# Kernel optimization log

Measured on AMD Instinct MI355X. Metric: run time of the kernel, lower is better.

## Reference

```python
import jax, jax.numpy as jnp
import numpy as np

NEG_SLOPE = 0.01  # torch LeakyReLU default


def setup_inputs() -> dict:
    N, H, Da, A, E, T, M = 100000, 256, 128, 250000, 60000, 512, 20000
    key = jax.random.key(0)
    ks = jax.random.split(key, 10)
    inp = {
        "nodes_representations": jax.random.normal(ks[0], (N, H), dtype=jnp.float32),
        "hyperedge_arg_node_idxs": jax.random.randint(ks[1], (A,), 0, N),
        "unq_hyperedge_type_reprs": jax.random.normal(ks[2], (T, H), dtype=jnp.float32),
        "hyperedge_type_name_unq_idxs": jax.random.randint(ks[3], (E,), 0, T),
        "unq_hyperedge_arg_name_reprs": jax.random.normal(ks[4], (M, Da), dtype=jnp.float32),
        "hyperedge_arg_name_unq_idxs": jax.random.randint(ks[5], (A,), 0, M),
        "hyperedge_arg_to_edge_id": jax.random.randint(ks[6], (A,), 0, E),
        "num_edges": E,
        "W1": jax.random.normal(ks[7], (H + Da, H), dtype=jnp.float32) * 0.05,
        "b1": jnp.zeros((H,), dtype=jnp.float32),
        "W2": jax.random.normal(ks[8], (2 * H + Da, H), dtype=jnp.float32) * 0.05,
        "b2": jnp.zeros((H,), dtype=jnp.float32),
    }
    return inp


def reference(nodes_representations, hyperedge_arg_node_idxs, unq_hyperedge_type_reprs,
              hyperedge_type_name_unq_idxs, unq_hyperedge_arg_name_reprs,
              hyperedge_arg_name_unq_idxs, hyperedge_arg_to_edge_id, num_edges,
              W1, b1, W2, b2):
    # Gather per-arg name and node reprs, concat -> [A, Da+H]
    arg_name = unq_hyperedge_arg_name_reprs[hyperedge_arg_name_unq_idxs]
    arg_node = nodes_representations[hyperedge_arg_node_idxs]
    arg_reprs = jnp.concatenate([arg_name, arg_node], axis=-1)

    Da = arg_name.shape[1]
    # Edge type reprs [E, H], zero-padded to [E, H+Da] (branch always taken here)
    edge_type = unq_hyperedge_type_reprs[hyperedge_type_name_unq_idxs]
    edge_type = jnp.concatenate(
        [edge_type, jnp.zeros((edge_type.shape[0], Da), dtype=edge_type.dtype)], axis=-1)

    # Message MLP on stacked [A+E, H+Da]
    all_in = jnp.concatenate([arg_reprs, edge_type], axis=0)
    msgs = jax.nn.leaky_relu(all_in @ W1 + b1, negative_slope=NEG_SLOPE)

    # Segment-max grouped by edge id (every edge gets its own type message, so no empty segments)
    seg_ids = jnp.concatenate(
        [hyperedge_arg_to_edge_id, jnp.arange(num_edges, dtype=hyperedge_arg_to_edge_id.dtype)])
    edge_states = jax.ops.segment_max(msgs, seg_ids, num_segments=num_edges)

    # Update MLP: gather edge state per arg, concat with arg reprs -> [A, 2H+Da]
    # (Dropout is identity in eval mode.)
    upd_in = jnp.concatenate([edge_states[hyperedge_arg_to_edge_id], arg_reprs], axis=1)
    message_to_nodes = jax.nn.leaky_relu(upd_in @ W2 + b2, negative_slope=NEG_SLOPE)
    return (message_to_nodes, edge_states)
```

## Files before the change

kernel.cpp:

```cpp
#include <hip/hip_runtime.h>
#include <stdint.h>

#define A_CNT 250000
#define E_CNT 60000
#define H_DIM 256
#define DA    128
#define K1    384
#define K2    640
#define NEG_SLOPE 0.01f
#define SENT  0xFFFFFFFFu
#define XS    40

typedef float v4f __attribute__((ext_vector_type(4)));
typedef short v8s __attribute__((ext_vector_type(8)));
typedef unsigned short u16;

__device__ __forceinline__ unsigned enc_f(float f) {
    unsigned u = __float_as_uint(f);
    return (u & 0x80000000u) ? ~u : (u | 0x80000000u);
}
__device__ __forceinline__ float dec_f(unsigned e) {
    unsigned u = (e & 0x80000000u) ? (e & 0x7FFFFFFFu) : ~e;
    return __uint_as_float(u);
}
__device__ __forceinline__ u16 f2bf(float f) {
    unsigned u = __float_as_uint(f);
    u += 0x7FFFu + ((u >> 16) & 1u);
    return (u16)(u >> 16);
}
__device__ __forceinline__ uint4 pack8(float4 a, float4 b) {
    union { u16 u[8]; uint4 v; } p;
    p.u[0]=f2bf(a.x); p.u[1]=f2bf(a.y); p.u[2]=f2bf(a.z); p.u[3]=f2bf(a.w);
    p.u[4]=f2bf(b.x); p.u[5]=f2bf(b.y); p.u[6]=f2bf(b.z); p.u[7]=f2bf(b.w);
    return p.v;
}

__global__ void wprep_kernel(const float* __restrict__ W, u16* __restrict__ Wt, int K) {
    int k = blockIdx.x, c = threadIdx.x;
    Wt[(size_t)c * K + k] = f2bf(W[(size_t)k * 256 + c]);
}

__global__ void hist_kernel(const int* __restrict__ arg_edge, unsigned* __restrict__ counts) {
    int i = blockIdx.x * 256 + threadIdx.x;
    if (i < A_CNT) atomicAdd(&counts[arg_edge[i]], 1u);
}

__global__ __launch_bounds__(1024) void scan_kernel(const unsigned* __restrict__ counts,
                                                    unsigned* __restrict__ cursor) {
    __shared__ unsigned sd[1024];
    const int tid = threadIdx.x;
    const int CH = (E_CNT + 1023) / 1024;
    const int base = tid * CH;
    unsigned s = 0;
    for (int i = 0; i < CH; ++i) { int idx = base + i; if (idx < E_CNT) s += counts[idx]; }
    sd[tid] = s; __syncthreads();
    for (int d = 1; d < 1024; d <<= 1) {
        unsigned v = (tid >= d) ? sd[tid - d] : 0u; __syncthreads();
        sd[tid] += v; __syncthreads();
    }
    unsigned run = sd[tid] - s;
    for (int i = 0; i < CH; ++i) {
        int idx = base + i;
        if (idx < E_CNT) { cursor[idx] = run; run += counts[idx]; }
    }
}

__global__ void scatter_kernel(const int* __restrict__ arg_edge, unsigned* __restrict__ cursor,
                               unsigned* __restrict__ perm, unsigned* __restrict__ sorted_edge) {
    int i = blockIdx.x * 256 + threadIdx.x;
    if (i < A_CNT) {
        int e = arg_edge[i];
        unsigned pos = atomicAdd(&cursor[e], 1u);
        perm[pos] = (unsigned)i;
        sorted_edge[pos] = (unsigned)e;
    }
}

__global__ __launch_bounds__(256, 3) void gemm1_kernel(
    const float* __restrict__ nodes, const int* __restrict__ arg_node_idx,
    const float* __restrict__ types, const int* __restrict__ type_idx,
    const float* __restrict__ names, const int* __restrict__ arg_name_idx,
    const unsigned* __restrict__ perm, const unsigned* __restrict__ sorted_edge,
    const u16* __restrict__ Wt1, const float* __restrict__ b1,
    unsigned* __restrict__ enc)
{
    __shared__ __align__(16) u16 sX[128 * XS];
    __shared__ __align__(16) u16 sW[128 * XS];
    const int t = threadIdx.x;
    const int row0 = blockIdx.x * 128;
    const int col0 = blockIdx.y * 128;

    const int srow = t >> 1, half = t & 1;
    const int gr = row0 + srow;
    const float* base0 = nullptr; const float* base1 = nullptr;
    if (gr < A_CNT) {
        int aid = (int)perm[gr];
        base0 = names + (size_t)arg_name_idx[aid] * DA;
        base1 = nodes + (size_t)arg_node_idx[aid] * H_DIM;
    } else if (gr < A_CNT + E_CNT) {
        base0 = types + (size_t)type_idx[gr - A_CNT] * H_DIM;
    }
    const u16* wrow = Wt1 + (size_t)(col0 + srow) * K1;

    const int lane = t & 63, wave = t >> 6;
    const int wr = (wave & 1) * 64, wc = (wave >> 1) * 64;
    const int lm = lane & 15, lq = lane >> 4;

    v4f acc[4][4];
    #pragma unroll
    for (int i = 0; i < 4; ++i)
        #pragma unroll
        for (int j = 0; j < 4; ++j) acc[i][j] = (v4f)0.f;

    for (int kc = 0; kc < K1; kc += 32) {
        const int k = kc + half * 16;
        float4 f0 = {0,0,0,0}, f1 = f0, f2 = f0, f3 = f0;
        if (gr < A_CNT) {
            const float* p = (k < DA) ? (base0 + k) : (base1 + (k - DA));
            f0 = ((const float4*)p)[0]; f1 = ((const float4*)p)[1];
            f2 = ((const float4*)p)[2]; f3 = ((const float4*)p)[3];
        } else if (gr < A_CNT + E_CNT && k < H_DIM) {
            const float* p = base0 + k;
            f0 = ((const float4*)p)[0]; f1 = ((const float4*)p)[1];
            f2 = ((const float4*)p)[2]; f3 = ((const float4*)p)[3];
        }
        uint4* xdst = (uint4*)&sX[srow * XS + half * 16];
        xdst[0] = pack8(f0, f1); xdst[1] = pack8(f2, f3);
        const uint4* wsrc = (const uint4*)(wrow + kc + half * 16);
        uint4 w0 = wsrc[0], w1 = wsrc[1];
        uint4* wdst = (uint4*)&sW[srow * XS + half * 16];
        wdst[0] = w0; wdst[1] = w1;
        __syncthreads();

        v8s af[4], bf[4];
        #pragma unroll
        for (int i = 0; i < 4; ++i) af[i] = *(const v8s*)&sX[(wr + i*16 + lm) * XS + lq * 8];
        #pragma unroll
        for (int j = 0; j < 4; ++j) bf[j] = *(const v8s*)&sW[(wc + j*16 + lm) * XS + lq * 8];
        #pragma unroll
        for (int i = 0; i < 4; ++i)
            #pragma unroll
            for (int j = 0; j < 4; ++j)
                acc[i][j] = __builtin_amdgcn_mfma_f32_16x16x32_bf16(af[i], bf[j], acc[i][j], 0, 0, 0);
        __syncthreads();
    }

    float bb[4];
    #pragma unroll
    for (int j = 0; j < 4; ++j) bb[j] = b1[col0 + wc + j*16 + lm];

    #pragma unroll
    for (int i = 0; i < 4; ++i) {
        const int r0 = row0 + wr + i*16 + lq*4;
        unsigned seg[4];
        #pragma unroll
        for (int reg = 0; reg < 4; ++reg) {
            int g = r0 + reg;
            seg[reg] = (g < A_CNT) ? sorted_edge[g]
                     : (g < A_CNT + E_CNT ? (unsigned)(g - A_CNT) : SENT);
        }
        #pragma unroll
        for (int j = 0; j < 4; ++j) {
            const int cj = col0 + wc + j*16 + lm;
            float v[4];
            #pragma unroll
            for (int reg = 0; reg < 4; ++reg) {
                float y = acc[i][j][reg] + bb[j];
                v[reg] = (y >= 0.f) ? y : NEG_SLOPE * y;
            }
            unsigned cs = seg[0]; float m = v[0];
            #pragma unroll
            for (int reg = 1; reg < 4; ++reg) {
                if (seg[reg] == cs) { m = fmaxf(m, v[reg]); }
                else {
                    if (cs != SENT) atomicMax(&enc[(size_t)cs * H_DIM + cj], enc_f(m));
                    cs = seg[reg]; m = v[reg];
                }
            }
            if (cs != SENT) atomicMax(&enc[(size_t)cs * H_DIM + cj], enc_f(m));
        }
    }
}

__global__ void decode_kernel(unsigned* __restrict__ enc, u16* __restrict__ es_bf) {
    size_t i = (size_t)blockIdx.x * 1024 + threadIdx.x;
    if (i < (size_t)E_CNT * H_DIM) {
        float f = dec_f(enc[i]);
        ((float*)enc)[i] = f;
        es_bf[i] = f2bf(f);
    }
}

__global__ __launch_bounds__(256, 3) void gemm2_kernel(
    const float* __restrict__ nodes, const int* __restrict__ arg_node_idx,
    const float* __restrict__ names, const int* __restrict__ arg_name_idx,
    const int* __restrict__ arg_edge, const u16* __restrict__ es_bf,
    const u16* __restrict__ Wt2, const float* __restrict__ b2,
    float* __restrict__ out)
{
    __shared__ __align__(16) u16 sX[128 * XS];
    __shared__ __align__(16) u16 sW[128 * XS];
    const int t = threadIdx.x;
    const int row0 = blockIdx.x * 128;
    const int col0 = blockIdx.y * 128;

    const int srow = t >> 1, half = t & 1;
    const int gr = row0 + srow;
    const u16* baseE = nullptr; const float* baseN = nullptr; const float* baseD = nullptr;
    if (gr < A_CNT) {
        baseE = es_bf + (size_t)arg_edge[gr] * H_DIM;
        baseN = names + (size_t)arg_name_idx[gr] * DA;
        baseD = nodes + (size_t)arg_node_idx[gr] * H_DIM;
    }
    const u16* wrow = Wt2 + (size_t)(col0 + srow) * K2;

    const int lane = t & 63, wave = t >> 6;
    const int wr = (wave & 1) * 64, wc = (wave >> 1) * 64;
    const int lm = lane & 15, lq = lane >> 4;

    v4f acc[4][4];
    #pragma unroll
    for (int i = 0; i < 4; ++i)
        #pragma unroll
        for (int j = 0; j < 4; ++j) acc[i][j] = (v4f)0.f;

    for (int kc = 0; kc < K2; kc += 32) {
        const int k = kc + half * 16;
        uint4 x0 = {0,0,0,0}, x1 = {0,0,0,0};
        if (gr < A_CNT) {
            if (k < H_DIM) {
                const uint4* p = (const uint4*)(baseE + k);
                x0 = p[0]; x1 = p[1];
            } else {
                const float* p = (k < H_DIM + DA) ? (baseN + (k - H_DIM))
                                                  : (baseD + (k - H_DIM - DA));
                float4 f0 = ((const float4*)p)[0], f1 = ((const float4*)p)[1];
                float4 f2 = ((const float4*)p)[2], f3 = ((const float4*)p)[3];
                x0 = pack8(f0, f1); x1 = pack8(f2, f3);
            }
        }
        uint4* xdst = (uint4*)&sX[srow * XS + half * 16];
        xdst[0] = x0; xdst[1] = x1;
        const uint4* wsrc = (const uint4*)(wrow + kc + half * 16);
        uint4 w0 = wsrc[0], w1 = wsrc[1];
        uint4* wdst = (uint4*)&sW[srow * XS + half * 16];
        wdst[0] = w0; wdst[1] = w1;
        __syncthreads();

        v8s af[4], bf[4];
        #pragma unroll
        for (int i = 0; i < 4; ++i) af[i] = *(const v8s*)&sX[(wr + i*16 + lm) * XS + lq * 8];
        #pragma unroll
        for (int j = 0; j < 4; ++j) bf[j] = *(const v8s*)&sW[(wc + j*16 + lm) * XS + lq * 8];
        #pragma unroll
        for (int i = 0; i < 4; ++i)
            #pragma unroll
            for (int j = 0; j < 4; ++j)
                acc[i][j] = __builtin_amdgcn_mfma_f32_16x16x32_bf16(af[i], bf[j], acc[i][j], 0, 0, 0);
        __syncthreads();
    }

    float bb[4];
    #pragma unroll
    for (int j = 0; j < 4; ++j) bb[j] = b2[col0 + wc + j*16 + lm];

    #pragma unroll
    for (int i = 0; i < 4; ++i) {
        const int r0 = row0 + wr + i*16 + lq*4;
        #pragma unroll
        for (int reg = 0; reg < 4; ++reg) {
            const int g = r0 + reg;
            if (g < A_CNT) {
                #pragma unroll
                for (int j = 0; j < 4; ++j) {
                    float y = acc[i][j][reg] + bb[j];
                    y = (y >= 0.f) ? y : NEG_SLOPE * y;
                    out[(size_t)g * H_DIM + col0 + wc + j*16 + lm] = y;
                }
            }
        }
    }
}

extern "C" void kernel_launch(void* const* d_in, const int* in_sizes, int n_in,
                              void* d_out, int out_size, void* d_ws, size_t ws_size,
                              hipStream_t stream) {
    const float* nodes        = (const float*)d_in[0];
    const int*   arg_node_idx = (const int*)  d_in[1];
    const float* types        = (const float*)d_in[2];
    const int*   type_idx     = (const int*)  d_in[3];
    const float* names        = (const float*)d_in[4];
    const int*   arg_name_idx = (const int*)  d_in[5];
    const int*   arg_edge     = (const int*)  d_in[6];
    const float* W1           = (const float*)d_in[8];
    const float* b1           = (const float*)d_in[9];
    const float* W2           = (const float*)d_in[10];
    const float* b2           = (const float*)d_in[11];

    float* out_msg = (float*)d_out;
    float* out_es  = out_msg + (size_t)A_CNT * H_DIM;
    unsigned* enc  = (unsigned*)out_es;

    char* ws = (char*)d_ws;
    size_t off = 0;
    auto alloc = [&](size_t bytes) -> void* {
        void* p = ws + off;
        off = (off + bytes + 255) & ~(size_t)255;
        return p;
    };
    u16* Wt1          = (u16*)alloc((size_t)256 * K1 * sizeof(u16));
    u16* Wt2          = (u16*)alloc((size_t)256 * K2 * sizeof(u16));
    u16* es_bf        = (u16*)alloc((size_t)E_CNT * H_DIM * sizeof(u16));
    unsigned* counts  = (unsigned*)alloc((size_t)E_CNT * sizeof(unsigned));
    unsigned* cursor  = (unsigned*)alloc((size_t)E_CNT * sizeof(unsigned));
    unsigned* perm    = (unsigned*)alloc((size_t)A_CNT * sizeof(unsigned));
    unsigned* sorted_edge = (unsigned*)alloc((size_t)A_CNT * sizeof(unsigned));

    hipMemsetAsync(counts, 0, (size_t)E_CNT * sizeof(unsigned), stream);
    hipMemsetAsync(enc, 0, (size_t)E_CNT * H_DIM * sizeof(unsigned), stream);

    wprep_kernel<<<K1, 256, 0, stream>>>(W1, Wt1, K1);
    wprep_kernel<<<K2, 256, 0, stream>>>(W2, Wt2, K2);
    hist_kernel<<<(A_CNT + 255) / 256, 256, 0, stream>>>(arg_edge, counts);
    scan_kernel<<<1, 1024, 0, stream>>>(counts, cursor);
    scatter_kernel<<<(A_CNT + 255) / 256, 256, 0, stream>>>(arg_edge, cursor, perm, sorted_edge);

    dim3 g1((A_CNT + E_CNT + 127) / 128, 2);
    gemm1_kernel<<<g1, 256, 0, stream>>>(nodes, arg_node_idx, types, type_idx,
                                         names, arg_name_idx, perm, sorted_edge,
                                         Wt1, b1, enc);
    decode_kernel<<<(E_CNT * H_DIM + 1023) / 1024, 1024, 0, stream>>>(enc, es_bf);

    dim3 g2((A_CNT + 127) / 128, 2);
    gemm2_kernel<<<g2, 256, 0, stream>>>(nodes, arg_node_idx, names, arg_name_idx,
                                         arg_edge, es_bf, Wt2, b2, out_msg);
}
```

Before: 950.4 us.

## Pre-convert tables to bf16 and stage GEMM tiles via direct global-to-LDS loads

Node, name and type tables are converted to bf16 once up front. Both GEMM kernels then load their gathered rows straight into LDS with global_load_lds, using an XOR-swizzled unpadded layout in place of the padded register-staged path. This halves the bytes gathered from the tables in each GEMM, which happen twice per row across the two column blocks, and removes the per-tile fp32-to-bf16 packing from the GEMM loops. The decode kernel is also vectorised to four elements per thread. In exchange it adds conversion passes and workspace for the bf16 copies, relies on the swizzle being correct, and uses a zero buffer for padding.

```diff
diff --git a/kernel.cpp b/kernel.cpp
--- a/kernel.cpp
+++ b/kernel.cpp
@@ -3,13 +3,15 @@
 
 #define A_CNT 250000
 #define E_CNT 60000
+#define N_NODES 100000
+#define M_NAMES 20000
+#define T_TYPES 512
 #define H_DIM 256
 #define DA    128
 #define K1    384
 #define K2    640
 #define NEG_SLOPE 0.01f
 #define SENT  0xFFFFFFFFu
-#define XS    40
 
 typedef float v4f __attribute__((ext_vector_type(4)));
 typedef short v8s __attribute__((ext_vector_type(8)));
@@ -35,9 +37,24 @@
     return p.v;
 }
 
+__device__ __forceinline__ void gload16(const u16* g, u16* l) {
+    __builtin_amdgcn_global_load_lds(
+        (const __attribute__((address_space(1))) unsigned int*)(g),
+        (__attribute__((address_space(3))) unsigned int*)(l), 16, 0, 0);
+}
+
 __global__ void wprep_kernel(const float* __restrict__ W, u16* __restrict__ Wt, int K) {
     int k = blockIdx.x, c = threadIdx.x;
     Wt[(size_t)c * K + k] = f2bf(W[(size_t)k * 256 + c]);
+}
+
+__global__ void tobf16_kernel(const float* __restrict__ in, u16* __restrict__ out, int n8) {
+    int i = blockIdx.x * 256 + threadIdx.x;
+    if (i < n8) {
+        const float4* p = (const float4*)in + (size_t)2 * i;
+        float4 a = p[0], b = p[1];
+        ((uint4*)out)[i] = pack8(a, b);
+    }
 }
 
 __global__ void hist_kernel(const int* __restrict__ arg_edge, unsigned* __restrict__ counts) {
@@ -77,35 +94,61 @@
 }
 
 __global__ __launch_bounds__(256, 3) void gemm1_kernel(
-    const float* __restrict__ nodes, const int* __restrict__ arg_node_idx,
-    const float* __restrict__ types, const int* __restrict__ type_idx,
-    const float* __restrict__ names, const int* __restrict__ arg_name_idx,
+    const u16* __restrict__ nodes_bf, const int* __restrict__ arg_node_idx,
+    const u16* __restrict__ types_bf, const int* __restrict__ type_idx,
+    const u16* __restrict__ names_bf, const int* __restrict__ arg_name_idx,
     const unsigned* __restrict__ perm, const unsigned* __restrict__ sorted_edge,
     const u16* __restrict__ Wt1, const float* __restrict__ b1,
+    const u16* __restrict__ zbuf,
     unsigned* __restrict__ enc)
 {
-    __shared__ __align__(16) u16 sX[128 * XS];
-    __shared__ __align__(16) u16 sW[128 * XS];
+    __shared__ __align__(16) u16 sX[128 * 32];
+    __shared__ __align__(16) u16 sW[128 * 32];
     const int t = threadIdx.x;
+    const int lane = t & 63, wave = t >> 6;
     const int row0 = blockIdx.x * 128;
     const int col0 = blockIdx.y * 128;
 
-    const int srow = t >> 1, half = t & 1;
-    const int gr = row0 + srow;
-    const float* base0 = nullptr; const float* base1 = nullptr;
-    if (gr < A_CNT) {
-        int aid = (int)perm[gr];
-        base0 = names + (size_t)arg_name_idx[aid] * DA;
-        base1 = nodes + (size_t)arg_node_idx[aid] * H_DIM;
-    } else if (gr < A_CNT + E_CNT) {
-        base0 = types + (size_t)type_idx[gr - A_CNT] * H_DIM;
-    }
-    const u16* wrow = Wt1 + (size_t)(col0 + srow) * K1;
-
-    const int lane = t & 63, wave = t >> 6;
+    const int rsub = wave * 16 + (lane >> 2);
+    const int slot = lane & 3;
+
+    const u16* xs0[2]; const u16* xs1[2]; int xcls[2];
+    const u16* ws[2];
+    u16* xdst[2]; u16* wdst[2];
+    #pragma unroll
+    for (int c = 0; c < 2; ++c) {
+        const int rloc = c * 64 + rsub;
+        const int ss = slot ^ ((rloc >> 1) & 3);
+        const int gr = row0 + rloc;
+        if (gr < A_CNT) {
+            int aid = (int)perm[gr];
+            xcls[c] = 0;
+            xs0[c] = names_bf + (size_t)arg_name_idx[aid] * DA + ss * 8;
+            xs1[c] = nodes_bf + (size_t)arg_node_idx[aid] * H_DIM + ss * 8 - DA;
+        } else if (gr < A_CNT + E_CNT) {
+            xcls[c] = 1;
+            xs0[c] = types_bf + (size_t)type_idx[gr - A_CNT] * H_DIM + ss * 8;
+            xs1[c] = zbuf;
+        } else {
+            xcls[c] = 2; xs0[c] = zbuf; xs1[c] = zbuf;
+        }
+        ws[c]   = Wt1 + (size_t)(col0 + rloc) * K1 + ss * 8;
+        xdst[c] = &sX[(c * 64 + wave * 16) * 32];
+        wdst[c] = &sW[(c * 64 + wave * 16) * 32];
+    }
+
     const int wr = (wave & 1) * 64, wc = (wave >> 1) * 64;
     const int lm = lane & 15, lq = lane >> 4;
 
+    int xoff[4], woff[4];
+    #pragma unroll
+    for (int i = 0; i < 4; ++i) {
+        int ra = wr + i * 16 + lm;
+        xoff[i] = ra * 32 + (lq ^ ((ra >> 1) & 3)) * 8;
+        int rb = wc + i * 16 + lm;
+        woff[i] = rb * 32 + (lq ^ ((rb >> 1) & 3)) * 8;
+    }
+
     v4f acc[4][4];
     #pragma unroll
     for (int i = 0; i < 4; ++i)
@@ -113,30 +156,22 @@
         for (int j = 0; j < 4; ++j) acc[i][j] = (v4f)0.f;
 
     for (int kc = 0; kc < K1; kc += 32) {
-        const int k = kc + half * 16;
-        float4 f0 = {0,0,0,0}, f1 = f0, f2 = f0, f3 = f0;
-        if (gr < A_CNT) {
-            const float* p = (k < DA) ? (base0 + k) : (base1 + (k - DA));
-            f0 = ((const float4*)p)[0]; f1 = ((const float4*)p)[1];
-            f2 = ((const float4*)p)[2]; f3 = ((const float4*)p)[3];
-        } else if (gr < A_CNT + E_CNT && k < H_DIM) {
-            const float* p = base0 + k;
-            f0 = ((const float4*)p)[0]; f1 = ((const float4*)p)[1];
-            f2 = ((const float4*)p)[2]; f3 = ((const float4*)p)[3];
-        }
-        uint4* xdst = (uint4*)&sX[srow * XS + half * 16];
-        xdst[0] = pack8(f0, f1); xdst[1] = pack8(f2, f3);
-        const uint4* wsrc = (const uint4*)(wrow + kc + half * 16);
-        uint4 w0 = wsrc[0], w1 = wsrc[1];
-        uint4* wdst = (uint4*)&sW[srow * XS + half * 16];
-        wdst[0] = w0; wdst[1] = w1;
+        #pragma unroll
+        for (int c = 0; c < 2; ++c) {
+            const u16* xsrc;
+            if (xcls[c] == 0)      xsrc = ((kc < DA) ? xs0[c] : xs1[c]) + kc;
+            else if (xcls[c] == 1) xsrc = (kc < H_DIM) ? (xs0[c] + kc) : zbuf;
+            else                   xsrc = zbuf;
+            gload16(xsrc, xdst[c]);
+            gload16(ws[c] + kc, wdst[c]);
+        }
         __syncthreads();
 
         v8s af[4], bf[4];
         #pragma unroll
-        for (int i = 0; i < 4; ++i) af[i] = *(const v8s*)&sX[(wr + i*16 + lm) * XS + lq * 8];
-        #pragma unroll
-        for (int j = 0; j < 4; ++j) bf[j] = *(const v8s*)&sW[(wc + j*16 + lm) * XS + lq * 8];
+        for (int i = 0; i < 4; ++i) af[i] = *(const v8s*)&sX[xoff[i]];
+        #pragma unroll
+        for (int j = 0; j < 4; ++j) bf[j] = *(const v8s*)&sW[woff[j]];
         #pragma unroll
         for (int i = 0; i < 4; ++i)
             #pragma unroll
@@ -184,40 +219,69 @@
 
 __global__ void decode_kernel(unsigned* __restrict__ enc, u16* __restrict__ es_bf) {
     size_t i = (size_t)blockIdx.x * 1024 + threadIdx.x;
-    if (i < (size_t)E_CNT * H_DIM) {
-        float f = dec_f(enc[i]);
-        ((float*)enc)[i] = f;
-        es_bf[i] = f2bf(f);
+    const size_t n4 = (size_t)E_CNT * H_DIM / 4;
+    if (i < n4) {
+        uint4 e = ((const uint4*)enc)[i];
+        float4 f;
+        f.x = dec_f(e.x); f.y = dec_f(e.y); f.z = dec_f(e.z); f.w = dec_f(e.w);
+        ((float4*)enc)[i] = f;
+        union { u16 u[4]; unsigned long long v; } p;
+        p.u[0]=f2bf(f.x); p.u[1]=f2bf(f.y); p.u[2]=f2bf(f.z); p.u[3]=f2bf(f.w);
+        ((unsigned long long*)es_bf)[i] = p.v;
     }
 }
 
 __global__ __launch_bounds__(256, 3) void gemm2_kernel(
-    const float* __restrict__ nodes, const int* __restrict__ arg_node_idx,
-    const float* __restrict__ names, const int* __restrict__ arg_name_idx,
+    const u16* __restrict__ nodes_bf, const int* __restrict__ arg_node_idx,
+    const u16* __restrict__ names_bf, const int* __restrict__ arg_name_idx,
     const int* __restrict__ arg_edge, const u16* __restrict__ es_bf,
     const u16* __restrict__ Wt2, const float* __restrict__ b2,
+    const u16* __restrict__ zbuf,
     float* __restrict__ out)
 {
-    __shared__ __align__(16) u16 sX[128 * XS];
-    __shared__ __align__(16) u16 sW[128 * XS];
+    __shared__ __align__(16) u16 sX[128 * 32];
+    __shared__ __align__(16) u16 sW[128 * 32];
     const int t = threadIdx.x;
+    const int lane = t & 63, wave = t >> 6;
     const int row0 = blockIdx.x * 128;
     const int col0 = blockIdx.y * 128;
 
-    const int srow = t >> 1, half = t & 1;
-    const int gr = row0 + srow;
-    const u16* baseE = nullptr; const float* baseN = nullptr; const float* baseD = nullptr;
-    if (gr < A_CNT) {
-        baseE = es_bf + (size_t)arg_edge[gr] * H_DIM;
-        baseN = names + (size_t)arg_name_idx[gr] * DA;
-        baseD = nodes + (size_t)arg_node_idx[gr] * H_DIM;
-    }
-    const u16* wrow = Wt2 + (size_t)(col0 + srow) * K2;
-
-    const int lane = t & 63, wave = t >> 6;
+    const int rsub = wave * 16 + (lane >> 2);
+    const int slot = lane & 3;
+
+    const u16* pe[2]; const u16* pn[2]; const u16* pd[2]; int valid[2];
+    const u16* ws[2];
+    u16* xdst[2]; u16* wdst[2];
+    #pragma unroll
+    for (int c = 0; c < 2; ++c) {
+        const int rloc = c * 64 + rsub;
+        const int ss = slot ^ ((rloc >> 1) & 3);
+        const int gr = row0 + rloc;
+        if (gr < A_CNT) {
+            valid[c] = 1;
+            pe[c] = es_bf   + (size_t)arg_edge[gr]      * H_DIM + ss * 8;
+            pn[c] = names_bf + (size_t)arg_name_idx[gr] * DA    + ss * 8 - H_DIM;
+            pd[c] = nodes_bf + (size_t)arg_node_idx[gr] * H_DIM + ss * 8 - H_DIM - DA;
+        } else {
+            valid[c] = 0; pe[c] = zbuf; pn[c] = zbuf; pd[c] = zbuf;
+        }
+        ws[c]   = Wt2 + (size_t)(col0 + rloc) * K2 + ss * 8;
+        xdst[c] = &sX[(c * 64 + wave * 16) * 32];
+        wdst[c] = &sW[(c * 64 + wave * 16) * 32];
+    }
+
     const int wr = (wave & 1) * 64, wc = (wave >> 1) * 64;
     const int lm = lane & 15, lq = lane >> 4;
 
+    int xoff[4], woff[4];
+    #pragma unroll
+    for (int i = 0; i < 4; ++i) {
+        int ra = wr + i * 16 + lm;
+        xoff[i] = ra * 32 + (lq ^ ((ra >> 1) & 3)) * 8;
+        int rb = wc + i * 16 + lm;
+        woff[i] = rb * 32 + (lq ^ ((rb >> 1) & 3)) * 8;
+    }
+
     v4f acc[4][4];
     #pragma unroll
     for (int i = 0; i < 4; ++i)
@@ -225,33 +289,23 @@
         for (int j = 0; j < 4; ++j) acc[i][j] = (v4f)0.f;
 
     for (int kc = 0; kc < K2; kc += 32) {
-        const int k = kc + half * 16;
-        uint4 x0 = {0,0,0,0}, x1 = {0,0,0,0};
-        if (gr < A_CNT) {
-            if (k < H_DIM) {
-                const uint4* p = (const uint4*)(baseE + k);
-                x0 = p[0]; x1 = p[1];
-            } else {
-                const float* p = (k < H_DIM + DA) ? (baseN + (k - H_DIM))
-                                                  : (baseD + (k - H_DIM - DA));
-                float4 f0 = ((const float4*)p)[0], f1 = ((const float4*)p)[1];
-                float4 f2 = ((const float4*)p)[2], f3 = ((const float4*)p)[3];
-                x0 = pack8(f0, f1); x1 = pack8(f2, f3);
-            }
-        }
-        uint4* xdst = (uint4*)&sX[srow * XS + half * 16];
-        xdst[0] = x0; xdst[1] = x1;
-        const uint4* wsrc = (const uint4*)(wrow + kc + half * 16);
-        uint4 w0 = wsrc[0], w1 = wsrc[1];
-        uint4* wdst = (uint4*)&sW[srow * XS + half * 16];
-        wdst[0] = w0; wdst[1] = w1;
+        #pragma unroll
+        for (int c = 0; c < 2; ++c) {
+            const u16* xsrc;
+            if (valid[c]) {
+                const u16* p = (kc < H_DIM) ? pe[c] : ((kc < H_DIM + DA) ? pn[c] : pd[c]);
+                xsrc = p + kc;
+            } else xsrc = zbuf;
+            gload16(xsrc, xdst[c]);
+            gload16(ws[c] + kc, wdst[c]);
+        }
         __syncthreads();
 
         v8s af[4], bf[4];
         #pragma unroll
-        for (int i = 0; i < 4; ++i) af[i] = *(const v8s*)&sX[(wr + i*16 + lm) * XS + lq * 8];
-        #pragma unroll
-        for (int j = 0; j < 4; ++j) bf[j] = *(const v8s*)&sW[(wc + j*16 + lm) * XS + lq * 8];
+        for (int i = 0; i < 4; ++i) af[i] = *(const v8s*)&sX[xoff[i]];
+        #pragma unroll
+        for (int j = 0; j < 4; ++j) bf[j] = *(const v8s*)&sW[woff[j]];
         #pragma unroll
         for (int i = 0; i < 4; ++i)
             #pragma unroll
@@ -311,6 +365,10 @@
     u16* Wt1          = (u16*)alloc((size_t)256 * K1 * sizeof(u16));
     u16* Wt2          = (u16*)alloc((size_t)256 * K2 * sizeof(u16));
     u16* es_bf        = (u16*)alloc((size_t)E_CNT * H_DIM * sizeof(u16));
+    u16* nodes_bf     = (u16*)alloc((size_t)N_NODES * H_DIM * sizeof(u16));
+    u16* names_bf     = (u16*)alloc((size_t)M_NAMES * DA * sizeof(u16));
+    u16* types_bf     = (u16*)alloc((size_t)T_TYPES * H_DIM * sizeof(u16));
+    u16* zbuf         = (u16*)alloc(256);
     unsigned* counts  = (unsigned*)alloc((size_t)E_CNT * sizeof(unsigned));
     unsigned* cursor  = (unsigned*)alloc((size_t)E_CNT * sizeof(unsigned));
     unsigned* perm    = (unsigned*)alloc((size_t)A_CNT * sizeof(unsigned));
@@ -318,20 +376,33 @@
 
     hipMemsetAsync(counts, 0, (size_t)E_CNT * sizeof(unsigned), stream);
     hipMemsetAsync(enc, 0, (size_t)E_CNT * H_DIM * sizeof(unsigned), stream);
+    hipMemsetAsync(zbuf, 0, 256, stream);
 
     wprep_kernel<<<K1, 256, 0, stream>>>(W1, Wt1, K1);
     wprep_kernel<<<K2, 256, 0, stream>>>(W2, Wt2, K2);
+    {
+        int n8 = N_NODES * H_DIM / 8;
+        tobf16_kernel<<<(n8 + 255) / 256, 256, 0, stream>>>(nodes, nodes_bf, n8);
+    }
+    {
+        int n8 = M_NAMES * DA / 8;
+        tobf16_kernel<<<(n8 + 255) / 256, 256, 0, stream>>>(names, names_bf, n8);
+    }
+    {
+        int n8 = T_TYPES * H_DIM / 8;
+        tobf16_kernel<<<(n8 + 255) / 256, 256, 0, stream>>>(types, types_bf, n8);
+    }
     hist_kernel<<<(A_CNT + 255) / 256, 256, 0, stream>>>(arg_edge, counts);
     scan_kernel<<<1, 1024, 0, stream>>>(counts, cursor);
     scatter_kernel<<<(A_CNT + 255) / 256, 256, 0, stream>>>(arg_edge, cursor, perm, sorted_edge);
 
     dim3 g1((A_CNT + E_CNT + 127) / 128, 2);
-    gemm1_kernel<<<g1, 256, 0, stream>>>(nodes, arg_node_idx, types, type_idx,
-                                         names, arg_name_idx, perm, sorted_edge,
-                                         Wt1, b1, enc);
-    decode_kernel<<<(E_CNT * H_DIM + 1023) / 1024, 1024, 0, stream>>>(enc, es_bf);
+    gemm1_kernel<<<g1, 256, 0, stream>>>(nodes_bf, arg_node_idx, types_bf, type_idx,
+                                         names_bf, arg_name_idx, perm, sorted_edge,
+                                         Wt1, b1, zbuf, enc);
+    decode_kernel<<<((E_CNT * H_DIM / 4) + 1023) / 1024, 1024, 0, stream>>>(enc, es_bf);
 
     dim3 g2((A_CNT + 127) / 128, 2);
-    gemm2_kernel<<<g2, 256, 0, stream>>>(nodes, arg_node_idx, names, arg_name_idx,
-                                         arg_edge, es_bf, Wt2, b2, out_msg);
-}
+    gemm2_kernel<<<g2, 256, 0, stream>>>(nodes_bf, arg_node_idx, names_bf, arg_name_idx,
+                                         arg_edge, es_bf, Wt2, b2, zbuf, out_msg);
+}
```

Result: faster. 877.2 us (-7.7%).
